# Kernel optimization log

Measured on AMD Instinct MI355X. Metric: run time of the kernel, lower is better.

Reference implementation:

```python
import jax, jax.numpy as jnp
import numpy as np

D_K = 64  # head dim used for scaling, matches init d_k


def setup_inputs() -> dict:
    key = jax.random.key(0)
    k1, k2, k3 = jax.random.split(key, 3)
    shape = (2, 2048, 16, 64)  # [batch, seq, heads, head_dim]
    q = jax.random.normal(k1, shape, dtype=jnp.float32)
    k = jax.random.normal(k2, shape, dtype=jnp.float32)
    v = jax.random.normal(k3, shape, dtype=jnp.float32)
    return {"q": q, "k": k, "v": v}


def reference(q, k, v):
    # score: [n, h, q, k]
    scale = 1.0 / np.sqrt(D_K).astype(np.float32)
    score = jnp.einsum('nqhd,nkhd->nhqk', q, k) * scale
    attn = jax.nn.softmax(score, axis=-1)
    context = jnp.einsum('nhqk,nkhd->nqhd', attn, v)
    return (context, attn)
```

## Files before the change

kernel.cpp:

```cpp
#include <hip/hip_runtime.h>

#define BATCH 2
#define SEQ   2048
#define NH    16
#define HD    64
#define RS    (NH*HD)
#define NPAIR (BATCH*NH)
#define NKT   (SEQ/64)
#define TILE_SHORTS 4096

typedef float f32x4  __attribute__((ext_vector_type(4)));
typedef short short8 __attribute__((ext_vector_type(8)));

#define GAS __attribute__((address_space(1)))
#define LAS __attribute__((address_space(3)))
#define DRAIN() asm volatile("s_waitcnt vmcnt(0)" ::: "memory")

__device__ __forceinline__ unsigned f2bf(float f) {
    union { float f; unsigned u; } c; c.f = f;
    return (c.u + 0x7FFFu + ((c.u >> 16) & 1u)) >> 16;
}
__device__ __forceinline__ unsigned pk(float lo, float hi) {
    return f2bf(lo) | (f2bf(hi) << 16);
}
__device__ __forceinline__ int swz(int row, int bc) {
    return (row * 128 + bc) ^ ((row & 7) << 4);
}
__device__ __forceinline__ short8 lds16(const void* p) {
    union { uint4 u; short8 s; } cv;
    cv.u = *(const uint4*)p;
    return cv.s;
}

extern "C" __global__ __launch_bounds__(256)
void pack_kv(const float* __restrict__ k, const float* __restrict__ v,
             unsigned short* __restrict__ ktl, unsigned short* __restrict__ vtl)
{
    __shared__ float Vf[64 * 65];
    const int bid = blockIdx.x;
    const int tid = threadIdx.x;

    if (bid < NPAIR * NKT) {
        const int kti = bid & 31, h = (bid >> 5) & 15, n = bid >> 9;
        const float* Kg = k + (((long)n * SEQ + kti * 64) * NH + h) * HD;
        char* out = (char*)(ktl + (long)bid * TILE_SHORTS);
        #pragma unroll
        for (int i = 0; i < 2; ++i) {
            int cid = tid + i * 256;
            int row = cid >> 3, cg = cid & 7;
            const float* src = Kg + row * RS + cg * 8;
            float4 f0 = *(const float4*)src;
            float4 f1 = *(const float4*)(src + 4);
            uint4 o = { pk(f0.x, f0.y), pk(f0.z, f0.w), pk(f1.x, f1.y), pk(f1.z, f1.w) };
            *(uint4*)(out + swz(row, cg * 16)) = o;
        }
    } else {
        const int b2 = bid - NPAIR * NKT;
        const int kti = b2 & 31, h = (b2 >> 5) & 15, n = b2 >> 9;
        const float* Vg = v + (((long)n * SEQ + kti * 64) * NH + h) * HD;
        #pragma unroll
        for (int i = 0; i < 4; ++i) {
            int idx = tid + i * 256;
            int row = idx >> 4, c4 = idx & 15;
            float4 f = *(const float4*)(Vg + row * RS + c4 * 4);
            Vf[row * 65 + c4 * 4 + 0] = f.x;
            Vf[row * 65 + c4 * 4 + 1] = f.y;
            Vf[row * 65 + c4 * 4 + 2] = f.z;
            Vf[row * 65 + c4 * 4 + 3] = f.w;
        }
        __syncthreads();
        char* out = (char*)(vtl + (long)b2 * TILE_SHORTS);
        #pragma unroll
        for (int i = 0; i < 2; ++i) {
            int cid = tid + i * 256;
            int d = cid >> 3, cg = cid & 7;
            float a0 = Vf[(cg * 8 + 0) * 65 + d], a1 = Vf[(cg * 8 + 1) * 65 + d];
            float a2 = Vf[(cg * 8 + 2) * 65 + d], a3 = Vf[(cg * 8 + 3) * 65 + d];
            float a4 = Vf[(cg * 8 + 4) * 65 + d], a5 = Vf[(cg * 8 + 5) * 65 + d];
            float a6 = Vf[(cg * 8 + 6) * 65 + d], a7 = Vf[(cg * 8 + 7) * 65 + d];
            uint4 o = { pk(a0, a1), pk(a2, a3), pk(a4, a5), pk(a6, a7) };
            *(uint4*)(out + swz(d, cg * 16)) = o;
        }
    }
}

extern "C" __global__ __launch_bounds__(256, 4)
void sdpa_kernel(const float* __restrict__ q,
                 const unsigned short* __restrict__ ktl,
                 const unsigned short* __restrict__ vtl,
                 float* __restrict__ ctx, float* __restrict__ attn,
                 int skip_pair)
{
    __shared__ unsigned short Kd[2][TILE_SHORTS];
    __shared__ unsigned short Vd[2][TILE_SHORTS];
    __shared__ unsigned short Ps[4][1024];

    const int bid = blockIdx.x;
    const int qt = bid & 31, pair = bid >> 5;
    const int h = pair & 15, n = pair >> 4;
    const int tid = threadIdx.x;
    const int w = tid >> 6, lane = tid & 63, lh = lane & 15, ks = lane >> 4;
    const bool wattn = (pair != skip_pair);

    const float* Qr = q + (((long)n * SEQ + qt * 64 + w * 16 + lh) * NH + h) * HD;
    short8 bq0, bq1;
    {
        union { unsigned u[4]; short8 s; } t;
        float4 f0 = *(const float4*)(Qr + ks * 8);
        float4 f1 = *(const float4*)(Qr + ks * 8 + 4);
        t.u[0] = pk(f0.x * 0.125f, f0.y * 0.125f);
        t.u[1] = pk(f0.z * 0.125f, f0.w * 0.125f);
        t.u[2] = pk(f1.x * 0.125f, f1.y * 0.125f);
        t.u[3] = pk(f1.z * 0.125f, f1.w * 0.125f);
        bq0 = t.s;
        float4 g0 = *(const float4*)(Qr + 32 + ks * 8);
        float4 g1 = *(const float4*)(Qr + 32 + ks * 8 + 4);
        t.u[0] = pk(g0.x * 0.125f, g0.y * 0.125f);
        t.u[1] = pk(g0.z * 0.125f, g0.w * 0.125f);
        t.u[2] = pk(g1.x * 0.125f, g1.y * 0.125f);
        t.u[3] = pk(g1.z * 0.125f, g1.w * 0.125f);
        bq1 = t.s;
    }

    const unsigned short* Ktile = ktl + (long)pair * NKT * TILE_SHORTS;
    const unsigned short* Vtile = vtl + (long)pair * NKT * TILE_SHORTS;

    auto stage = [&](unsigned short* lbuf, const unsigned short* gt) {
        #pragma unroll
        for (int i = 0; i < 2; ++i) {
            const unsigned short* g = gt + w * 1024 + i * 512 + lane * 8;
            unsigned short* l = lbuf + w * 1024 + i * 512;
            __builtin_amdgcn_global_load_lds((const GAS unsigned int*)g,
                                             (LAS unsigned int*)l, 16, 0, 0);
        }
    };

    stage(Kd[0], Ktile);
    DRAIN();
    __syncthreads();
    float lsum = 0.f;
    for (int kt = 0; kt < NKT; ++kt) {
        const int cur = kt & 1;
        if (kt < NKT - 1) stage(Kd[cur ^ 1], Ktile + (kt + 1) * TILE_SHORTS);
        const char* Kb = (const char*)Kd[cur];
        #pragma unroll
        for (int c = 0; c < 4; ++c) {
            short8 a0 = lds16(Kb + swz(c * 16 + lh, ks * 16));
            short8 a1 = lds16(Kb + swz(c * 16 + lh, 64 + ks * 16));
            f32x4 z = {0.f, 0.f, 0.f, 0.f};
            z = __builtin_amdgcn_mfma_f32_16x16x32_bf16(a0, bq0, z, 0, 0, 0);
            z = __builtin_amdgcn_mfma_f32_16x16x32_bf16(a1, bq1, z, 0, 0, 0);
            lsum += __expf(z[0]) + __expf(z[1]) + __expf(z[2]) + __expf(z[3]);
        }
        DRAIN();
        __syncthreads();
    }
    lsum += __shfl_xor(lsum, 16);
    lsum += __shfl_xor(lsum, 32);
    const float linv = 1.0f / lsum;

    f32x4 oacc[4];
    #pragma unroll
    for (int cd = 0; cd < 4; ++cd) oacc[cd] = (f32x4){0.f, 0.f, 0.f, 0.f};

    float* attnW = attn + (((long)pair) * SEQ + qt * 64 + w * 16 + lh) * SEQ + ks * 4;
    char* Pw = (char*)Ps[w];

    stage(Kd[0], Ktile);
    stage(Vd[0], Vtile);
    DRAIN();
    __syncthreads();
    for (int kt = 0; kt < NKT; ++kt) {
        const int cur = kt & 1;
        if (kt < NKT - 1) {
            stage(Kd[cur ^ 1], Ktile + (kt + 1) * TILE_SHORTS);
            stage(Vd[cur ^ 1], Vtile + (kt + 1) * TILE_SHORTS);
        }
        const char* Kb = (const char*)Kd[cur];
        f32x4 s[4];
        #pragma unroll
        for (int c = 0; c < 4; ++c) {
            short8 a0 = lds16(Kb + swz(c * 16 + lh, ks * 16));
            short8 a1 = lds16(Kb + swz(c * 16 + lh, 64 + ks * 16));
            f32x4 z = {0.f, 0.f, 0.f, 0.f};
            z = __builtin_amdgcn_mfma_f32_16x16x32_bf16(a0, bq0, z, 0, 0, 0);
            z = __builtin_amdgcn_mfma_f32_16x16x32_bf16(a1, bq1, z, 0, 0, 0);
            s[c] = z;
        }
        #pragma unroll
        for (int c = 0; c < 4; ++c) {
            f32x4 pv;
            pv[0] = __expf(s[c][0]) * linv;
            pv[1] = __expf(s[c][1]) * linv;
            pv[2] = __expf(s[c][2]) * linv;
            pv[3] = __expf(s[c][3]) * linv;
            if (wattn) *(f32x4*)(attnW + (long)kt * 64 + c * 16) = pv;
            uint2 u2 = { pk(pv[0], pv[1]), pk(pv[2], pv[3]) };
            *(uint2*)(Pw + swz(lh, c * 32 + ks * 8)) = u2;
        }
        short8 pa0 = lds16(Pw + swz(lh, ks * 16));
        short8 pa1 = lds16(Pw + swz(lh, 64 + ks * 16));
        const char* Vb = (const char*)Vd[cur];
        #pragma unroll
        for (int cd = 0; cd < 4; ++cd) {
            short8 bv0 = lds16(Vb + swz(cd * 16 + lh, ks * 16));
            short8 bv1 = lds16(Vb + swz(cd * 16 + lh, 64 + ks * 16));
            oacc[cd] = __builtin_amdgcn_mfma_f32_16x16x32_bf16(pa0, bv0, oacc[cd], 0, 0, 0);
            oacc[cd] = __builtin_amdgcn_mfma_f32_16x16x32_bf16(pa1, bv1, oacc[cd], 0, 0, 0);
        }
        DRAIN();
        __syncthreads();
    }

    float* ctxW = ctx + (((long)n * SEQ + qt * 64 + w * 16 + ks * 4) * NH + h) * HD + lh;
    #pragma unroll
    for (int cd = 0; cd < 4; ++cd) {
        #pragma unroll
        for (int r = 0; r < 4; ++r) {
            ctxW[r * RS + cd * 16] = oacc[cd][r];
        }
    }
}

extern "C" __global__ __launch_bounds__(256, 4)
void attn_fill(const float* __restrict__ q, const float* __restrict__ k,
               float* __restrict__ attn, int pair)
{
    __shared__ unsigned short Ksh[TILE_SHORTS];
    const int n = pair >> 4, h = pair & 15;
    const int qt = blockIdx.x;
    const int tid = threadIdx.x;
    const int w = tid >> 6, lane = tid & 63, lh = lane & 15, ks = lane >> 4;

    const float* Qr = q + (((long)n * SEQ + qt * 64 + w * 16 + lh) * NH + h) * HD;
    short8 bq0, bq1;
    {
        union { unsigned u[4]; short8 s; } t;
        float4 f0 = *(const float4*)(Qr + ks * 8);
        float4 f1 = *(const float4*)(Qr + ks * 8 + 4);
        t.u[0] = pk(f0.x * 0.125f, f0.y * 0.125f);
        t.u[1] = pk(f0.z * 0.125f, f0.w * 0.125f);
        t.u[2] = pk(f1.x * 0.125f, f1.y * 0.125f);
        t.u[3] = pk(f1.z * 0.125f, f1.w * 0.125f);
        bq0 = t.s;
        float4 g0 = *(const float4*)(Qr + 32 + ks * 8);
        float4 g1 = *(const float4*)(Qr + 32 + ks * 8 + 4);
        t.u[0] = pk(g0.x * 0.125f, g0.y * 0.125f);
        t.u[1] = pk(g0.z * 0.125f, g0.w * 0.125f);
        t.u[2] = pk(g1.x * 0.125f, g1.y * 0.125f);
        t.u[3] = pk(g1.z * 0.125f, g1.w * 0.125f);
        bq1 = t.s;
    }

    const float* Kg = k + ((long)n * SEQ * NH + h) * HD;

    float lsum = 0.f;
    for (int kt = 0; kt < NKT; ++kt) {
        __syncthreads();
        #pragma unroll
        for (int i = 0; i < 2; ++i) {
            int cid = tid + i * 256;
            int row = cid >> 3, cg = cid & 7;
            const float* src = Kg + ((long)kt * 64 + row) * RS + cg * 8;
            float4 f0 = *(const float4*)src;
            float4 f1 = *(const float4*)(src + 4);
            uint4 o = { pk(f0.x, f0.y), pk(f0.z, f0.w), pk(f1.x, f1.y), pk(f1.z, f1.w) };
            *(uint4*)((char*)Ksh + swz(row, cg * 16)) = o;
        }
        __syncthreads();
        #pragma unroll
        for (int c = 0; c < 4; ++c) {
            short8 a0 = lds16((const char*)Ksh + swz(c * 16 + lh, ks * 16));
            short8 a1 = lds16((const char*)Ksh + swz(c * 16 + lh, 64 + ks * 16));
            f32x4 z = {0.f, 0.f, 0.f, 0.f};
            z = __builtin_amdgcn_mfma_f32_16x16x32_bf16(a0, bq0, z, 0, 0, 0);
            z = __builtin_amdgcn_mfma_f32_16x16x32_bf16(a1, bq1, z, 0, 0, 0);
            lsum += __expf(z[0]) + __expf(z[1]) + __expf(z[2]) + __expf(z[3]);
        }
    }
    lsum += __shfl_xor(lsum, 16);
    lsum += __shfl_xor(lsum, 32);
    const float linv = 1.0f / lsum;

    float* attnW = attn + (((long)pair) * SEQ + qt * 64 + w * 16 + lh) * SEQ + ks * 4;
    for (int kt = 0; kt < NKT; ++kt) {
        __syncthreads();
        #pragma unroll
        for (int i = 0; i < 2; ++i) {
            int cid = tid + i * 256;
            int row = cid >> 3, cg = cid & 7;
            const float* src = Kg + ((long)kt * 64 + row) * RS + cg * 8;
            float4 f0 = *(const float4*)src;
            float4 f1 = *(const float4*)(src + 4);
            uint4 o = { pk(f0.x, f0.y), pk(f0.z, f0.w), pk(f1.x, f1.y), pk(f1.z, f1.w) };
            *(uint4*)((char*)Ksh + swz(row, cg * 16)) = o;
        }
        __syncthreads();
        #pragma unroll
        for (int c = 0; c < 4; ++c) {
            short8 a0 = lds16((const char*)Ksh + swz(c * 16 + lh, ks * 16));
            short8 a1 = lds16((const char*)Ksh + swz(c * 16 + lh, 64 + ks * 16));
            f32x4 z = {0.f, 0.f, 0.f, 0.f};
            z = __builtin_amdgcn_mfma_f32_16x16x32_bf16(a0, bq0, z, 0, 0, 0);
            z = __builtin_amdgcn_mfma_f32_16x16x32_bf16(a1, bq1, z, 0, 0, 0);
            f32x4 pv;
            pv[0] = __expf(z[0]) * linv;
            pv[1] = __expf(z[1]) * linv;
            pv[2] = __expf(z[2]) * linv;
            pv[3] = __expf(z[3]) * linv;
            *(f32x4*)(attnW + (long)kt * 64 + c * 16) = pv;
        }
    }
}

extern "C" void kernel_launch(void* const* d_in, const int* in_sizes, int n_in,
                              void* d_out, int out_size, void* d_ws, size_t ws_size,
                              hipStream_t stream)
{
    const float* q = (const float*)d_in[0];
    const float* k = (const float*)d_in[1];
    const float* v = (const float*)d_in[2];
    float* ctx  = (float*)d_out;
    float* attn = ctx + (size_t)BATCH * SEQ * NH * HD;

    const size_t tiles_shorts = (size_t)NPAIR * NKT * TILE_SHORTS;
    const size_t ws_need = 2 * tiles_shorts * sizeof(unsigned short);

    unsigned short *ktl, *vtl;
    int skip;
    if (ws_size >= ws_need) {
        ktl = (unsigned short*)d_ws;
        vtl = ktl + tiles_shorts;
        skip = -1;
    } else {
        ktl = (unsigned short*)(attn + (size_t)(NPAIR - 1) * SEQ * SEQ);
        vtl = ktl + tiles_shorts;
        skip = NPAIR - 1;
    }

    hipLaunchKernelGGL(pack_kv, dim3(2 * NPAIR * NKT), dim3(256), 0, stream, k, v, ktl, vtl);
    hipLaunchKernelGGL(sdpa_kernel, dim3(NPAIR * NKT), dim3(256), 0, stream, q, ktl, vtl, ctx, attn, skip);
    if (skip >= 0) {
        hipLaunchKernelGGL(attn_fill, dim3(32), dim3(256), 0, stream, q, k, attn, skip);
    }
}
```

Before: 198.1 us.

## Pre-pack K/V in MFMA fragment order, read pass-one K directly from global

The packed K/V tiles are now written in the exact per-lane MFMA fragment order, so each lane reads contiguous 16-byte chunks instead of swizzled rows. The first softmax-denominator pass reads K straight from global or L2, dropping its LDS staging and barriers. The second pass uses non-temporal stores for the large attention matrix, a partial vmcnt wait so outstanding stores do not block the barrier, and a remapped block index to group blocks differently across the device. The risks are relying on the vmcnt(4) count to cover the LDS loads correctly, and losing LDS reuse in pass one, which now depends on cache hits.

```diff
diff --git a/kernel.cpp b/kernel.cpp
--- a/kernel.cpp
+++ b/kernel.cpp
@@ -14,7 +14,6 @@
 
 #define GAS __attribute__((address_space(1)))
 #define LAS __attribute__((address_space(3)))
-#define DRAIN() asm volatile("s_waitcnt vmcnt(0)" ::: "memory")
 
 __device__ __forceinline__ unsigned f2bf(float f) {
     union { float f; unsigned u; } c; c.f = f;
@@ -26,7 +25,7 @@
 __device__ __forceinline__ int swz(int row, int bc) {
     return (row * 128 + bc) ^ ((row & 7) << 4);
 }
-__device__ __forceinline__ short8 lds16(const void* p) {
+__device__ __forceinline__ short8 ld16(const void* p) {
     union { uint4 u; short8 s; } cv;
     cv.u = *(const uint4*)p;
     return cv.s;
@@ -43,16 +42,16 @@
     if (bid < NPAIR * NKT) {
         const int kti = bid & 31, h = (bid >> 5) & 15, n = bid >> 9;
         const float* Kg = k + (((long)n * SEQ + kti * 64) * NH + h) * HD;
-        char* out = (char*)(ktl + (long)bid * TILE_SHORTS);
-        #pragma unroll
-        for (int i = 0; i < 2; ++i) {
-            int cid = tid + i * 256;
-            int row = cid >> 3, cg = cid & 7;
-            const float* src = Kg + row * RS + cg * 8;
+        uint4* out = (uint4*)(ktl + (long)bid * TILE_SHORTS);
+        #pragma unroll
+        for (int i = 0; i < 2; ++i) {
+            int cidx = tid + i * 256;
+            int c = cidx >> 7, j = (cidx >> 6) & 1, l = cidx & 63;
+            const float* src = Kg + (c * 16 + (l & 15)) * RS + j * 32 + (l >> 4) * 8;
             float4 f0 = *(const float4*)src;
             float4 f1 = *(const float4*)(src + 4);
             uint4 o = { pk(f0.x, f0.y), pk(f0.z, f0.w), pk(f1.x, f1.y), pk(f1.z, f1.w) };
-            *(uint4*)(out + swz(row, cg * 16)) = o;
+            out[cidx] = o;
         }
     } else {
         const int b2 = bid - NPAIR * NKT;
@@ -69,17 +68,19 @@
             Vf[row * 65 + c4 * 4 + 3] = f.w;
         }
         __syncthreads();
-        char* out = (char*)(vtl + (long)b2 * TILE_SHORTS);
-        #pragma unroll
-        for (int i = 0; i < 2; ++i) {
-            int cid = tid + i * 256;
-            int d = cid >> 3, cg = cid & 7;
-            float a0 = Vf[(cg * 8 + 0) * 65 + d], a1 = Vf[(cg * 8 + 1) * 65 + d];
-            float a2 = Vf[(cg * 8 + 2) * 65 + d], a3 = Vf[(cg * 8 + 3) * 65 + d];
-            float a4 = Vf[(cg * 8 + 4) * 65 + d], a5 = Vf[(cg * 8 + 5) * 65 + d];
-            float a6 = Vf[(cg * 8 + 6) * 65 + d], a7 = Vf[(cg * 8 + 7) * 65 + d];
+        uint4* out = (uint4*)(vtl + (long)b2 * TILE_SHORTS);
+        #pragma unroll
+        for (int i = 0; i < 2; ++i) {
+            int cidx = tid + i * 256;
+            int c = cidx >> 7, j = (cidx >> 6) & 1, l = cidx & 63;
+            int d = c * 16 + (l & 15);
+            int kb = j * 32 + (l >> 4) * 8;
+            float a0 = Vf[(kb + 0) * 65 + d], a1 = Vf[(kb + 1) * 65 + d];
+            float a2 = Vf[(kb + 2) * 65 + d], a3 = Vf[(kb + 3) * 65 + d];
+            float a4 = Vf[(kb + 4) * 65 + d], a5 = Vf[(kb + 5) * 65 + d];
+            float a6 = Vf[(kb + 6) * 65 + d], a7 = Vf[(kb + 7) * 65 + d];
             uint4 o = { pk(a0, a1), pk(a2, a3), pk(a4, a5), pk(a6, a7) };
-            *(uint4*)(out + swz(d, cg * 16)) = o;
+            out[cidx] = o;
         }
     }
 }
@@ -95,7 +96,8 @@
     __shared__ unsigned short Vd[2][TILE_SHORTS];
     __shared__ unsigned short Ps[4][1024];
 
-    const int bid = blockIdx.x;
+    const int bid0 = blockIdx.x;
+    const int bid  = ((bid0 & 7) << 7) | (bid0 >> 3);
     const int qt = bid & 31, pair = bid >> 5;
     const int h = pair & 15, n = pair >> 4;
     const int tid = threadIdx.x;
@@ -135,25 +137,19 @@
         }
     };
 
-    stage(Kd[0], Ktile);
-    DRAIN();
-    __syncthreads();
     float lsum = 0.f;
+    #pragma unroll 2
     for (int kt = 0; kt < NKT; ++kt) {
-        const int cur = kt & 1;
-        if (kt < NKT - 1) stage(Kd[cur ^ 1], Ktile + (kt + 1) * TILE_SHORTS);
-        const char* Kb = (const char*)Kd[cur];
-        #pragma unroll
-        for (int c = 0; c < 4; ++c) {
-            short8 a0 = lds16(Kb + swz(c * 16 + lh, ks * 16));
-            short8 a1 = lds16(Kb + swz(c * 16 + lh, 64 + ks * 16));
+        const char* T = (const char*)(Ktile + (long)kt * TILE_SHORTS);
+        #pragma unroll
+        for (int c = 0; c < 4; ++c) {
+            short8 a0 = ld16(T + ((c * 2 + 0) * 64 + lane) * 16);
+            short8 a1 = ld16(T + ((c * 2 + 1) * 64 + lane) * 16);
             f32x4 z = {0.f, 0.f, 0.f, 0.f};
             z = __builtin_amdgcn_mfma_f32_16x16x32_bf16(a0, bq0, z, 0, 0, 0);
             z = __builtin_amdgcn_mfma_f32_16x16x32_bf16(a1, bq1, z, 0, 0, 0);
             lsum += __expf(z[0]) + __expf(z[1]) + __expf(z[2]) + __expf(z[3]);
         }
-        DRAIN();
-        __syncthreads();
     }
     lsum += __shfl_xor(lsum, 16);
     lsum += __shfl_xor(lsum, 32);
@@ -168,20 +164,23 @@
 
     stage(Kd[0], Ktile);
     stage(Vd[0], Vtile);
-    DRAIN();
-    __syncthreads();
+    asm volatile("s_waitcnt vmcnt(0)" ::: "memory");
+    __builtin_amdgcn_s_barrier();
+
     for (int kt = 0; kt < NKT; ++kt) {
         const int cur = kt & 1;
         if (kt < NKT - 1) {
             stage(Kd[cur ^ 1], Ktile + (kt + 1) * TILE_SHORTS);
             stage(Vd[cur ^ 1], Vtile + (kt + 1) * TILE_SHORTS);
         }
+        asm volatile("" ::: "memory");
+
         const char* Kb = (const char*)Kd[cur];
         f32x4 s[4];
         #pragma unroll
         for (int c = 0; c < 4; ++c) {
-            short8 a0 = lds16(Kb + swz(c * 16 + lh, ks * 16));
-            short8 a1 = lds16(Kb + swz(c * 16 + lh, 64 + ks * 16));
+            short8 a0 = ld16(Kb + ((c * 2 + 0) * 64 + lane) * 16);
+            short8 a1 = ld16(Kb + ((c * 2 + 1) * 64 + lane) * 16);
             f32x4 z = {0.f, 0.f, 0.f, 0.f};
             z = __builtin_amdgcn_mfma_f32_16x16x32_bf16(a0, bq0, z, 0, 0, 0);
             z = __builtin_amdgcn_mfma_f32_16x16x32_bf16(a1, bq1, z, 0, 0, 0);
@@ -194,22 +193,27 @@
             pv[1] = __expf(s[c][1]) * linv;
             pv[2] = __expf(s[c][2]) * linv;
             pv[3] = __expf(s[c][3]) * linv;
-            if (wattn) *(f32x4*)(attnW + (long)kt * 64 + c * 16) = pv;
+            if (wattn) {
+                __builtin_nontemporal_store(pv, (f32x4*)(attnW + (long)kt * 64 + c * 16));
+            }
             uint2 u2 = { pk(pv[0], pv[1]), pk(pv[2], pv[3]) };
             *(uint2*)(Pw + swz(lh, c * 32 + ks * 8)) = u2;
         }
-        short8 pa0 = lds16(Pw + swz(lh, ks * 16));
-        short8 pa1 = lds16(Pw + swz(lh, 64 + ks * 16));
+        short8 pa0 = ld16(Pw + swz(lh, ks * 16));
+        short8 pa1 = ld16(Pw + swz(lh, 64 + ks * 16));
         const char* Vb = (const char*)Vd[cur];
         #pragma unroll
         for (int cd = 0; cd < 4; ++cd) {
-            short8 bv0 = lds16(Vb + swz(cd * 16 + lh, ks * 16));
-            short8 bv1 = lds16(Vb + swz(cd * 16 + lh, 64 + ks * 16));
+            short8 bv0 = ld16(Vb + ((cd * 2 + 0) * 64 + lane) * 16);
+            short8 bv1 = ld16(Vb + ((cd * 2 + 1) * 64 + lane) * 16);
             oacc[cd] = __builtin_amdgcn_mfma_f32_16x16x32_bf16(pa0, bv0, oacc[cd], 0, 0, 0);
             oacc[cd] = __builtin_amdgcn_mfma_f32_16x16x32_bf16(pa1, bv1, oacc[cd], 0, 0, 0);
         }
-        DRAIN();
-        __syncthreads();
+        if (kt < NKT - 1) {
+            if (wattn) asm volatile("s_waitcnt vmcnt(4)" ::: "memory");
+            else       asm volatile("s_waitcnt vmcnt(0)" ::: "memory");
+            __builtin_amdgcn_s_barrier();
+        }
     }
 
     float* ctxW = ctx + (((long)n * SEQ + qt * 64 + w * 16 + ks * 4) * NH + h) * HD + lh;
@@ -259,19 +263,19 @@
         __syncthreads();
         #pragma unroll
         for (int i = 0; i < 2; ++i) {
-            int cid = tid + i * 256;
-            int row = cid >> 3, cg = cid & 7;
-            const float* src = Kg + ((long)kt * 64 + row) * RS + cg * 8;
+            int cidx = tid + i * 256;
+            int c = cidx >> 7, j = (cidx >> 6) & 1, l = cidx & 63;
+            const float* src = Kg + ((long)kt * 64 + c * 16 + (l & 15)) * RS + j * 32 + (l >> 4) * 8;
             float4 f0 = *(const float4*)src;
             float4 f1 = *(const float4*)(src + 4);
             uint4 o = { pk(f0.x, f0.y), pk(f0.z, f0.w), pk(f1.x, f1.y), pk(f1.z, f1.w) };
-            *(uint4*)((char*)Ksh + swz(row, cg * 16)) = o;
-        }
-        __syncthreads();
-        #pragma unroll
-        for (int c = 0; c < 4; ++c) {
-            short8 a0 = lds16((const char*)Ksh + swz(c * 16 + lh, ks * 16));
-            short8 a1 = lds16((const char*)Ksh + swz(c * 16 + lh, 64 + ks * 16));
+            *((uint4*)Ksh + cidx) = o;
+        }
+        __syncthreads();
+        #pragma unroll
+        for (int c = 0; c < 4; ++c) {
+            short8 a0 = ld16((const char*)Ksh + ((c * 2 + 0) * 64 + lane) * 16);
+            short8 a1 = ld16((const char*)Ksh + ((c * 2 + 1) * 64 + lane) * 16);
             f32x4 z = {0.f, 0.f, 0.f, 0.f};
             z = __builtin_amdgcn_mfma_f32_16x16x32_bf16(a0, bq0, z, 0, 0, 0);
             z = __builtin_amdgcn_mfma_f32_16x16x32_bf16(a1, bq1, z, 0, 0, 0);
@@ -287,19 +291,19 @@
         __syncthreads();
         #pragma unroll
         for (int i = 0; i < 2; ++i) {
-            int cid = tid + i * 256;
-            int row = cid >> 3, cg = cid & 7;
-            const float* src = Kg + ((long)kt * 64 + row) * RS + cg * 8;
+            int cidx = tid + i * 256;
+            int c = cidx >> 7, j = (cidx >> 6) & 1, l = cidx & 63;
+            const float* src = Kg + ((long)kt * 64 + c * 16 + (l & 15)) * RS + j * 32 + (l >> 4) * 8;
             float4 f0 = *(const float4*)src;
             float4 f1 = *(const float4*)(src + 4);
             uint4 o = { pk(f0.x, f0.y), pk(f0.z, f0.w), pk(f1.x, f1.y), pk(f1.z, f1.w) };
-            *(uint4*)((char*)Ksh + swz(row, cg * 16)) = o;
-        }
-        __syncthreads();
-        #pragma unroll
-        for (int c = 0; c < 4; ++c) {
-            short8 a0 = lds16((const char*)Ksh + swz(c * 16 + lh, ks * 16));
-            short8 a1 = lds16((const char*)Ksh + swz(c * 16 + lh, 64 + ks * 16));
+            *((uint4*)Ksh + cidx) = o;
+        }
+        __syncthreads();
+        #pragma unroll
+        for (int c = 0; c < 4; ++c) {
+            short8 a0 = ld16((const char*)Ksh + ((c * 2 + 0) * 64 + lane) * 16);
+            short8 a1 = ld16((const char*)Ksh + ((c * 2 + 1) * 64 + lane) * 16);
             f32x4 z = {0.f, 0.f, 0.f, 0.f};
             z = __builtin_amdgcn_mfma_f32_16x16x32_bf16(a0, bq0, z, 0, 0, 0);
             z = __builtin_amdgcn_mfma_f32_16x16x32_bf16(a1, bq1, z, 0, 0, 0);
```

New measurement: 208.0 us. 1.05x slower.
